# Kernel optimization log

Hardware: AMD Instinct MI355X
Metric: run time of the kernel (lower is better)

Reference implementation:

```python
import jax, jax.numpy as jnp
import numpy as np

NUM_ENT = 14541
NUM_REL = 474
D = 400
B = 32
N_CAND = 14505


def setup_inputs() -> dict:
    key = jax.random.key(0)
    k0, k1, k2, k4, k5 = jax.random.split(key, 5)
    return {
        "arg0_1": jax.random.normal(k0, (NUM_ENT, D), dtype=jnp.float32),   # entity embeddings
        "arg1_1": jax.random.normal(k1, (NUM_REL, D), dtype=jnp.float32),   # relation centers
        "arg2_1": jax.random.uniform(k2, (NUM_REL, D), dtype=jnp.float32),  # relation offsets (box widths)
        "arg3_1": jnp.ones((1,), dtype=jnp.float32),                        # margin gamma
        "arg4_1": jax.random.randint(k4, (B, 2), 0, NUM_REL),               # (head_id, rel_id) pairs
        "arg5_1": jax.random.randint(k5, (4, N_CAND), 0, NUM_ENT),          # candidate entity ids (row 0 used)
    }


def reference(arg0_1, arg1_1, arg2_1, arg3_1, arg4_1, arg5_1):
    # Gather heads / relation params
    head = arg0_1[arg4_1[:, 0]]            # [B, D]
    rel_c = arg1_1[arg4_1[:, 1]]           # [B, D]
    rel_o = arg2_1[arg4_1[:, 1]]           # [B, D]

    query = (head + rel_c)[:, None, :]     # [B, 1, D] box center
    offset = rel_o[:, None, :]             # [B, 1, D] box width

    # Candidate tail embeddings: only row 0 of arg5_1 is used in the graph
    cand = arg0_1[arg5_1[0].reshape(-1)][None, :, :]  # [1, N_CAND, D]

    d = jnp.abs(cand - query)                           # [B, N_CAND, D]
    dist_outside = jax.nn.relu(d - offset).sum(-1)      # [B, N_CAND]
    dist_inside = jnp.abs(jnp.minimum(d, offset)).sum(-1)

    return arg3_1 - dist_outside - 0.02 * dist_inside   # [B, N_CAND]
```

## Files before the change

kernel.cpp:

```cpp
#include <hip/hip_runtime.h>

#define DIM     400
#define NENT    14541
#define B       32
#define NCAND   14505
#define NROUND  3627
#define TSTRIPS 256
#define THREADS 256
#define CVTBLK  2841

typedef __attribute__((ext_vector_type(2))) _Float16 half2_t;

static __device__ __forceinline__ half2_t bch(unsigned u) {
    return __builtin_bit_cast(half2_t, u);
}
static __device__ __forceinline__ half2_t habs2(half2_t x) {
    unsigned u = __builtin_bit_cast(unsigned, x) & 0x7fff7fffu;
    return __builtin_bit_cast(half2_t, u);
}
static __device__ __forceinline__ unsigned pkh(float x, float y) {
    half2_t h;
    h.x = (_Float16)x;
    h.y = (_Float16)y;
    return __builtin_bit_cast(unsigned, h);
}
static __device__ __forceinline__ float dot2acc(half2_t m, float s) {
#if __has_builtin(__builtin_amdgcn_fdot2)
    const half2_t ones = {(_Float16)1.f, (_Float16)1.f};
    return __builtin_amdgcn_fdot2(m, ones, s, false);
#else
    return s + (float)m.x + (float)m.y;
#endif
}

__global__ void setup_kernel(const float* __restrict__ ent,
                             const float* __restrict__ relc,
                             const float* __restrict__ relo,
                             const float* __restrict__ onev,
                             const int*   __restrict__ pairs,
                             uint4* __restrict__ ent16,
                             _Float16* __restrict__ q16,
                             _Float16* __restrict__ o16,
                             float* __restrict__ baseg) {
    const int blk = blockIdx.x;
    const int tid = threadIdx.x;
    if (blk < CVTBLK) {
        const int TOT8 = NENT * DIM / 8;
        int i = blk * THREADS + tid;
        if (i >= TOT8) return;
        const float4* s4 = (const float4*)ent;
        float4 a = s4[2 * i], c = s4[2 * i + 1];
        uint4 d;
        d.x = pkh(a.x, a.y);
        d.y = pkh(a.z, a.w);
        d.z = pkh(c.x, c.y);
        d.w = pkh(c.z, c.w);
        ent16[i] = d;
    } else {
        const int b = blk - CVTBLK;
        const int h = pairs[2 * b + 0];
        const int r = pairs[2 * b + 1];
        float so = 0.f;
        for (int i = tid; i < DIM; i += THREADS) {
            float qv = ent[(size_t)h * DIM + i] + relc[(size_t)r * DIM + i];
            float ov = relo[(size_t)r * DIM + i];
            q16[(size_t)b * DIM + i] = (_Float16)qv;
            o16[(size_t)b * DIM + i] = (_Float16)(0.98f * ov);
            so += ov;
        }
        __shared__ float sred[4];
        for (int off = 32; off; off >>= 1) so += __shfl_down(so, off);
        if ((tid & 63) == 0) sred[tid >> 6] = so;
        __syncthreads();
        if (tid == 0)
            baseg[b] = onev[0] + 0.98f * (sred[0] + sred[1] + sred[2] + sred[3]);
    }
}

__global__ __launch_bounds__(THREADS, 2)
void score_f16(const uint4* __restrict__ ent16,
               const uint4* __restrict__ q16,
               const uint4* __restrict__ o16,
               const float* __restrict__ baseg,
               const int*   __restrict__ cidx,
               float* __restrict__ out) {
    const int fid  = blockIdx.x;
    const int xcd  = fid & 7;
    const int rest = fid >> 3;
    const int beta = rest & 3;
    const int tc   = rest >> 2;
    const int t    = xcd + 8 * tc;

    const int tid  = threadIdx.x;
    const int wid  = tid >> 6;
    const int lane = tid & 63;
    const int u    = lane & 15;
    const int g    = lane >> 4;
    const int b0   = __builtin_amdgcn_readfirstlane(8 * beta + 2 * wid);
    const int b1   = b0 + 1;

    const uint4* qa = q16 + (size_t)b0 * 50;
    const uint4* oa = o16 + (size_t)b0 * 50;
    const uint4* qc = q16 + (size_t)b1 * 50;
    const uint4* oc = o16 + (size_t)b1 * 50;

    uint4 q0[4], o0[4], q1[4], o1[4];
    q0[0] = qa[u]; q0[1] = qa[u + 16]; q0[2] = qa[u + 32];
    o0[0] = oa[u]; o0[1] = oa[u + 16]; o0[2] = oa[u + 32];
    q1[0] = qc[u]; q1[1] = qc[u + 16]; q1[2] = qc[u + 32];
    o1[0] = oc[u]; o1[1] = oc[u + 16]; o1[2] = oc[u + 32];
    q0[3] = q0[0]; o0[3] = o0[0]; q1[3] = q1[0]; o1[3] = o1[0];
    if (u < 2) {
        q0[3] = qa[48 + u]; o0[3] = oa[48 + u];
        q1[3] = qc[48 + u]; o1[3] = oc[48 + u];
    }
    const float base0 = baseg[b0];
    const float base1 = baseg[b1];

    const half2_t K002 = {(_Float16)0.02f, (_Float16)0.02f};

#define PAIR(cu, qu, ou, SS)                                    \
    {                                                           \
        half2_t cc_ = bch(cu), qq_ = bch(qu), oo_ = bch(ou);    \
        half2_t dd_ = cc_ - qq_;                                \
        half2_t aa_ = habs2(dd_);                               \
        half2_t ee_ = aa_ * K002 + oo_;                         \
        half2_t mm_ = __builtin_elementwise_max(aa_, ee_);      \
        SS = dot2acc(mm_, SS);                                  \
    }
#define PROC(C, Q, O, SA, SB)                                   \
    PAIR(C.x, Q.x, O.x, SA) PAIR(C.y, Q.y, O.y, SB)             \
    PAIR(C.z, Q.z, O.z, SA) PAIR(C.w, Q.w, O.w, SB)

    for (int rr = t; rr < NROUND; rr += 2 * TSTRIPS) {
        const int rr2   = rr + TSTRIPS;
        const int candA = 4 * rr + g;
        const int candB = 4 * rr2 + g;
        const int ciA = cidx[candA < NCAND ? candA : NCAND - 1];
        const int ciB = cidx[candB < NCAND ? candB : NCAND - 1];
        const uint4* pA = ent16 + (size_t)ciA * 50;
        const uint4* pB = ent16 + (size_t)ciB * 50;

        uint4 av0 = pA[u], av1 = pA[u + 16], av2 = pA[u + 32];
        uint4 bv0 = pB[u], bv1 = pB[u + 16], bv2 = pB[u + 32];
        uint4 av3, bv3;
        if (u < 2) { av3 = pA[48 + u]; bv3 = pB[48 + u]; }

        float sA00 = 0.f, sA01 = 0.f, sA10 = 0.f, sA11 = 0.f;
        float sB00 = 0.f, sB01 = 0.f, sB10 = 0.f, sB11 = 0.f;

        PROC(av0, q0[0], o0[0], sA00, sA01)
        PROC(av1, q0[1], o0[1], sA00, sA01)
        PROC(av2, q0[2], o0[2], sA00, sA01)
        PROC(av0, q1[0], o1[0], sA10, sA11)
        PROC(av1, q1[1], o1[1], sA10, sA11)
        PROC(av2, q1[2], o1[2], sA10, sA11)
        if (u < 2) {
            PROC(av3, q0[3], o0[3], sA00, sA01)
            PROC(av3, q1[3], o1[3], sA10, sA11)
        }
        PROC(bv0, q0[0], o0[0], sB00, sB01)
        PROC(bv1, q0[1], o0[1], sB00, sB01)
        PROC(bv2, q0[2], o0[2], sB00, sB01)
        PROC(bv0, q1[0], o1[0], sB10, sB11)
        PROC(bv1, q1[1], o1[1], sB10, sB11)
        PROC(bv2, q1[2], o1[2], sB10, sB11)
        if (u < 2) {
            PROC(bv3, q0[3], o0[3], sB00, sB01)
            PROC(bv3, q1[3], o1[3], sB10, sB11)
        }

        float sA0 = sA00 + sA01;
        float sA1 = sA10 + sA11;
        float sB0 = sB00 + sB01;
        float sB1 = sB10 + sB11;
        sA0 += __shfl_xor(sA0, 1); sA1 += __shfl_xor(sA1, 1);
        sB0 += __shfl_xor(sB0, 1); sB1 += __shfl_xor(sB1, 1);
        sA0 += __shfl_xor(sA0, 2); sA1 += __shfl_xor(sA1, 2);
        sB0 += __shfl_xor(sB0, 2); sB1 += __shfl_xor(sB1, 2);
        sA0 += __shfl_xor(sA0, 4); sA1 += __shfl_xor(sA1, 4);
        sB0 += __shfl_xor(sB0, 4); sB1 += __shfl_xor(sB1, 4);
        sA0 += __shfl_xor(sA0, 8); sA1 += __shfl_xor(sA1, 8);
        sB0 += __shfl_xor(sB0, 8); sB1 += __shfl_xor(sB1, 8);

        if (u == 0) {
            if (candA < NCAND) {
                out[(size_t)b0 * NCAND + candA] = base0 - sA0;
                out[(size_t)b1 * NCAND + candA] = base1 - sA1;
            }
            if (candB < NCAND) {
                out[(size_t)b0 * NCAND + candB] = base0 - sB0;
                out[(size_t)b1 * NCAND + candB] = base1 - sB1;
            }
        }
    }
#undef PROC
#undef PAIR
}

__global__ __launch_bounds__(THREADS, 2)
void score_f32(const float* __restrict__ ent,
               const float* __restrict__ relc,
               const float* __restrict__ relo,
               const float* __restrict__ onev,
               const int*   __restrict__ pairs,
               const int*   __restrict__ cidx,
               float* __restrict__ out) {
    const int fid  = blockIdx.x;
    const int xcd  = fid & 7;
    const int rest = fid >> 3;
    const int bq   = rest & 7;
    const int tc   = rest >> 3;
    const int t    = xcd + 8 * tc;

    const int tid  = threadIdx.x;
    const int lane = tid & 63;
    const int u    = lane & 15;
    const int g    = lane >> 4;
    const int b    = __builtin_amdgcn_readfirstlane(bq * 4 + (tid >> 6));

    const int hd = pairs[b * 2 + 0];
    const int rl = pairs[b * 2 + 1];
    const float4* hb = (const float4*)(ent  + (size_t)hd * DIM) + u;
    const float4* cb = (const float4*)(relc + (size_t)rl * DIM) + u;
    const float4* ob = (const float4*)(relo + (size_t)rl * DIM) + u;

    float4 q[7], o[7];
    float oa = 0.f;
#pragma unroll
    for (int k = 0; k < 6; ++k) {
        float4 h = hb[16 * k], c = cb[16 * k];
        q[k] = make_float4(h.x + c.x, h.y + c.y, h.z + c.z, h.w + c.w);
        o[k] = ob[16 * k];
        oa += o[k].x + o[k].y + o[k].z + o[k].w;
    }
    if (u < 4) {
        float4 h = hb[96], c = cb[96];
        q[6] = make_float4(h.x + c.x, h.y + c.y, h.z + c.z, h.w + c.w);
        o[6] = ob[96];
        oa += o[6].x + o[6].y + o[6].z + o[6].w;
    }
    oa += __shfl_xor(oa, 1);
    oa += __shfl_xor(oa, 2);
    oa += __shfl_xor(oa, 4);
    oa += __shfl_xor(oa, 8);
    const float base = onev[0] + 0.98f * oa;

    const float4* entu = (const float4*)ent + u;

#define E(vc, vq, vo, AM, AD)                     \
        {                                         \
            float d_ = (vc) - (vq);               \
            AM += fmaxf(fabsf(d_), (vo));         \
            AD += fabsf(d_);                      \
        }
#define F4(k, AM, AD)                             \
        E(cbuf[k].x, q[k].x, o[k].x, AM, AD)      \
        E(cbuf[k].y, q[k].y, o[k].y, AM, AD)      \
        E(cbuf[k].z, q[k].z, o[k].z, AM, AD)      \
        E(cbuf[k].w, q[k].w, o[k].w, AM, AD)

    for (int rr = t; rr < NROUND; rr += TSTRIPS) {
        const int cand = 4 * rr + g;
        const int ci   = cidx[cand < NCAND ? cand : NCAND - 1];
        const float4* p = entu + (size_t)ci * 100;

        float4 cbuf[7];
#pragma unroll
        for (int k = 0; k < 6; ++k) cbuf[k] = p[16 * k];
        if (u < 4) cbuf[6] = p[96];

        float am0 = 0.f, ad0 = 0.f, am1 = 0.f, ad1 = 0.f;
        F4(0, am0, ad0) F4(1, am1, ad1)
        F4(2, am0, ad0) F4(3, am1, ad1)
        F4(4, am0, ad0) F4(5, am1, ad1)
        if (u < 4) { F4(6, am0, ad0) }

        float s_ = fmaf(-0.98f, am0 + am1, -0.02f * (ad0 + ad1));
        s_ += __shfl_xor(s_, 1);
        s_ += __shfl_xor(s_, 2);
        s_ += __shfl_xor(s_, 4);
        s_ += __shfl_xor(s_, 8);

        if (u == 0 && cand < NCAND)
            out[(size_t)b * NCAND + cand] = base + s_;
    }
#undef F4
#undef E
}

extern "C" void kernel_launch(void* const* d_in, const int* in_sizes, int n_in,
                              void* d_out, int out_size, void* d_ws, size_t ws_size,
                              hipStream_t stream) {
    const float* ent   = (const float*)d_in[0];
    const float* relc  = (const float*)d_in[1];
    const float* relo  = (const float*)d_in[2];
    const float* onev  = (const float*)d_in[3];
    const int*   pairs = (const int*)d_in[4];
    const int*   cidx  = (const int*)d_in[5];
    float*       out   = (float*)d_out;

    const size_t entB = (size_t)NENT * DIM * 2;
    const size_t qB   = (size_t)B * DIM * 2;
    const size_t need = entB + 2 * qB + B * sizeof(float);

    if (ws_size >= need) {
        unsigned char* w = (unsigned char*)d_ws;
        uint4*    ent16 = (uint4*)w;
        _Float16* q16   = (_Float16*)(w + entB);
        _Float16* o16   = (_Float16*)(w + entB + qB);
        float*    baseg = (float*)(w + entB + 2 * qB);

        setup_kernel<<<CVTBLK + B, THREADS, 0, stream>>>(
            ent, relc, relo, onev, pairs, ent16, q16, o16, baseg);
        score_f16<<<8 * 4 * 32, THREADS, 0, stream>>>(
            ent16, (const uint4*)q16, (const uint4*)o16, baseg, cidx, out);
    } else {
        score_f32<<<8 * 8 * 32, THREADS, 0, stream>>>(
            ent, relc, relo, onev, pairs, cidx, out);
    }
}
```

Measured before the change: 42.20 us.

## Pre-gather candidate rows into dense fp16 buffer and assign contiguous row ranges

The setup kernel now gathers the candidate entity rows by index while converting to fp16, writing a dense buffer ordered by candidate. The scoring kernel then reads contiguous rows and gives each strip a contiguous block of rounds instead of a strided set, with no index lookup. This removes the per-round dependent index load and improves locality in the main kernel. In exchange the setup kernel does a gathered read, which may be less coalesced than the previous linear conversion pass.

```diff
diff --git a/kernel.cpp b/kernel.cpp
--- a/kernel.cpp
+++ b/kernel.cpp
@@ -5,9 +5,11 @@
 #define B       32
 #define NCAND   14505
 #define NROUND  3627
-#define TSTRIPS 256
+#define NSTRIPS 256
 #define THREADS 256
-#define CVTBLK  2841
+#define DROWS   14508
+#define CVTN    (DROWS * 50)
+#define CVTBLK  ((CVTN + THREADS - 1) / THREADS)
 
 typedef __attribute__((ext_vector_type(2))) _Float16 half2_t;
 
@@ -38,24 +40,28 @@
                              const float* __restrict__ relo,
                              const float* __restrict__ onev,
                              const int*   __restrict__ pairs,
-                             uint4* __restrict__ ent16,
+                             const int*   __restrict__ cidx,
+                             uint4* __restrict__ dense16,
                              _Float16* __restrict__ q16,
                              _Float16* __restrict__ o16,
                              float* __restrict__ baseg) {
     const int blk = blockIdx.x;
     const int tid = threadIdx.x;
     if (blk < CVTBLK) {
-        const int TOT8 = NENT * DIM / 8;
         int i = blk * THREADS + tid;
-        if (i >= TOT8) return;
-        const float4* s4 = (const float4*)ent;
-        float4 a = s4[2 * i], c = s4[2 * i + 1];
+        if (i >= CVTN) return;
+        int row = i / 50;
+        int col = i - row * 50;
+        int n  = row < NCAND ? row : NCAND - 1;
+        int ci = cidx[n];
+        const float4* s4 = (const float4*)(ent + (size_t)ci * DIM) + col * 2;
+        float4 a = s4[0], c = s4[1];
         uint4 d;
         d.x = pkh(a.x, a.y);
         d.y = pkh(a.z, a.w);
         d.z = pkh(c.x, c.y);
         d.w = pkh(c.z, c.w);
-        ent16[i] = d;
+        dense16[i] = d;
     } else {
         const int b = blk - CVTBLK;
         const int h = pairs[2 * b + 0];
@@ -78,18 +84,20 @@
 }
 
 __global__ __launch_bounds__(THREADS, 2)
-void score_f16(const uint4* __restrict__ ent16,
+void score_f16(const uint4* __restrict__ dense16,
                const uint4* __restrict__ q16,
                const uint4* __restrict__ o16,
                const float* __restrict__ baseg,
-               const int*   __restrict__ cidx,
                float* __restrict__ out) {
     const int fid  = blockIdx.x;
     const int xcd  = fid & 7;
     const int rest = fid >> 3;
     const int beta = rest & 3;
     const int tc   = rest >> 2;
-    const int t    = xcd + 8 * tc;
+    const int strip = xcd + 8 * tc;
+
+    const int r0 = strip * 14 + (strip < 43 ? strip : 43);
+    const int r1 = r0 + 14 + (strip < 43 ? 1 : 0);
 
     const int tid  = threadIdx.x;
     const int wid  = tid >> 6;
@@ -132,14 +140,11 @@
     PAIR(C.x, Q.x, O.x, SA) PAIR(C.y, Q.y, O.y, SB)             \
     PAIR(C.z, Q.z, O.z, SA) PAIR(C.w, Q.w, O.w, SB)
 
-    for (int rr = t; rr < NROUND; rr += 2 * TSTRIPS) {
-        const int rr2   = rr + TSTRIPS;
-        const int candA = 4 * rr + g;
-        const int candB = 4 * rr2 + g;
-        const int ciA = cidx[candA < NCAND ? candA : NCAND - 1];
-        const int ciB = cidx[candB < NCAND ? candB : NCAND - 1];
-        const uint4* pA = ent16 + (size_t)ciA * 50;
-        const uint4* pB = ent16 + (size_t)ciB * 50;
+    for (int rr = r0; rr < r1; rr += 2) {
+        const int rA = rr;
+        const int rB = (rr + 1 < r1) ? rr + 1 : rr;
+        const uint4* pA = dense16 + (size_t)(4 * rA + g) * 50;
+        const uint4* pB = dense16 + (size_t)(4 * rB + g) * 50;
 
         uint4 av0 = pA[u], av1 = pA[u + 16], av2 = pA[u + 32];
         uint4 bv0 = pB[u], bv1 = pB[u + 16], bv2 = pB[u + 32];
@@ -184,11 +189,13 @@
         sB0 += __shfl_xor(sB0, 8); sB1 += __shfl_xor(sB1, 8);
 
         if (u == 0) {
+            const int candA = 4 * rA + g;
+            const int candB = 4 * rB + g;
             if (candA < NCAND) {
                 out[(size_t)b0 * NCAND + candA] = base0 - sA0;
                 out[(size_t)b1 * NCAND + candA] = base1 - sA1;
             }
-            if (candB < NCAND) {
+            if (rB != rA && candB < NCAND) {
                 out[(size_t)b0 * NCAND + candB] = base0 - sB0;
                 out[(size_t)b1 * NCAND + candB] = base1 - sB1;
             }
@@ -260,7 +267,7 @@
         E(cbuf[k].z, q[k].z, o[k].z, AM, AD)      \
         E(cbuf[k].w, q[k].w, o[k].w, AM, AD)
 
-    for (int rr = t; rr < NROUND; rr += TSTRIPS) {
+    for (int rr = t; rr < NROUND; rr += NSTRIPS) {
         const int cand = 4 * rr + g;
         const int ci   = cidx[cand < NCAND ? cand : NCAND - 1];
         const float4* p = entu + (size_t)ci * 100;
@@ -300,21 +307,21 @@
     const int*   cidx  = (const int*)d_in[5];
     float*       out   = (float*)d_out;
 
-    const size_t entB = (size_t)NENT * DIM * 2;
+    const size_t denB = (size_t)DROWS * DIM * 2;
     const size_t qB   = (size_t)B * DIM * 2;
-    const size_t need = entB + 2 * qB + B * sizeof(float);
+    const size_t need = denB + 2 * qB + B * sizeof(float);
 
     if (ws_size >= need) {
         unsigned char* w = (unsigned char*)d_ws;
-        uint4*    ent16 = (uint4*)w;
-        _Float16* q16   = (_Float16*)(w + entB);
-        _Float16* o16   = (_Float16*)(w + entB + qB);
-        float*    baseg = (float*)(w + entB + 2 * qB);
+        uint4*    dense16 = (uint4*)w;
+        _Float16* q16     = (_Float16*)(w + denB);
+        _Float16* o16     = (_Float16*)(w + denB + qB);
+        float*    baseg   = (float*)(w + denB + 2 * qB);
 
         setup_kernel<<<CVTBLK + B, THREADS, 0, stream>>>(
-            ent, relc, relo, onev, pairs, ent16, q16, o16, baseg);
+            ent, relc, relo, onev, pairs, cidx, dense16, q16, o16, baseg);
         score_f16<<<8 * 4 * 32, THREADS, 0, stream>>>(
-            ent16, (const uint4*)q16, (const uint4*)o16, baseg, cidx, out);
+            dense16, (const uint4*)q16, (const uint4*)o16, baseg, out);
     } else {
         score_f32<<<8 * 8 * 32, THREADS, 0, stream>>>(
             ent, relc, relo, onev, pairs, cidx, out);
```

Measured after the change: 39.84 us. 1.06x faster.
